# Performance work log

Hardware: AMD Instinct MI355X
Metric: run time of the kernel (lower is better)

The kernel has to match this reference:

```python
import jax, jax.numpy as jnp
import numpy as np

N_NODES = 500_000
N_HYPER = 5_000_000
N_ADJ = 16_000_000


def setup_inputs() -> dict:
    key = jax.random.key(0)
    k1, k2, k3 = jax.random.split(key, 3)
    x = jax.random.uniform(k1, (N_NODES,), dtype=jnp.float32)
    hyper_edges = jax.random.randint(k2, (N_HYPER, 3), 0, N_NODES, dtype=jnp.int32)
    adj_edges = jax.random.randint(k3, (N_ADJ, 2), 0, N_NODES, dtype=jnp.int32)
    return {"x": x, "t": 0, "hyper_edges": hyper_edges, "adj_edges": adj_edges}


def reference(x, t, hyper_edges, adj_edges):
    # x: [N] node states; hyper_edges: [E,3] size-3 hyperedges; adj_edges: [M,2] (src,dst)
    N = x.shape[0]

    # --- hyperedge gather-product-scatter (update_result_3, vectorized) ---
    xe = x[hyper_edges]                       # [E,3] gathered member states
    prod = xe[:, 1] * xe[:, 2]                # product over nodes[1:]
    vals = prod[:, None] - xe * xe            # [E,3] per-member contribution
    hyper_res = jax.ops.segment_sum(
        vals.reshape(-1), hyper_edges.reshape(-1), num_segments=N)

    # --- sparse Laplacian SpMV: L@x = deg*x - A@x (edge-list form) ---
    src = adj_edges[:, 0]
    dst = adj_edges[:, 1]
    Ax = jax.ops.segment_sum(x[src], dst, num_segments=N)
    deg = jax.ops.segment_sum(jnp.ones_like(src, dtype=x.dtype), dst, num_segments=N)
    Lx = deg * x - Ax

    # forward: -0.1 * L@x + 0.9 * hyperedge result
    return -0.1 * Lx + 0.9 * hyper_res
```

## Files before the change

kernel.cpp:

```cpp
#include <hip/hip_runtime.h>
#include <hip/hip_fp16.h>


#define W_BUCKET   8192
#define W_SHIFT    13
#define NB_MAX     62
#define S_STAGE    128
#define A_THREADS  512
#define A_BLOCKS   1024
#define ADJ_TILE   6144
#define HYP_TILE   2048
#define B_PB       16
#define CAP_A      262144
#define CAP_H      245760
#define SRC_MASK   0x7FFFFu

typedef int      v4i __attribute__((ext_vector_type(4)));
typedef unsigned v4u __attribute__((ext_vector_type(4)));
typedef float    v4f __attribute__((ext_vector_type(4)));

#define NT_LOAD(p)     __builtin_nontemporal_load(p)
#define NT_STORE(v, p) __builtin_nontemporal_store((v), (p))


__global__ __launch_bounds__(256) void zero_f4_kernel(float4* __restrict__ p, long long n4) {
    long long tid = (long long)blockIdx.x * blockDim.x + threadIdx.x;
    long long stride = (long long)gridDim.x * blockDim.x;
    for (long long i = tid; i < n4; i += stride) p[i] = make_float4(0.f, 0.f, 0.f, 0.f);
}

__global__ __launch_bounds__(256) void fused_scatter_kernel(
    const float* __restrict__ x, const int2* __restrict__ adj,
    const int* __restrict__ hyper, float* __restrict__ out,
    int n_adj, int n_hyper)
{
    const long long tid = (long long)blockIdx.x * blockDim.x + threadIdx.x;
    const long long stride = (long long)gridDim.x * blockDim.x;
    for (long long i = tid; i < n_adj; i += stride) {
        int2 e = adj[i];
        atomicAdd(&out[e.y], 0.1f * (x[e.x] - x[e.y]));
    }
    for (long long i = tid; i < n_hyper; i += stride) {
        int i0 = hyper[3*i], i1 = hyper[3*i+1], i2 = hyper[3*i+2];
        float x0 = x[i0], x1 = x[i1], x2 = x[i2];
        float p = x1 * x2;
        atomicAdd(&out[i0], 0.9f * (p - x0*x0));
        atomicAdd(&out[i1], 0.9f * (p - x1*x1));
        atomicAdd(&out[i2], 0.9f * (p - x2*x2));
    }
}


__global__ __launch_bounds__(256) void zero_int_kernel(int* __restrict__ p, int n) {
    int tid = blockIdx.x * blockDim.x + threadIdx.x;
    int stride = gridDim.x * blockDim.x;
    for (int i = tid; i < n; i += stride) p[i] = 0;
}


template <int KIND>
__device__ __forceinline__ void flush_stage(int nb, int* cur, int* basev, int* cnts,
                                            unsigned int* stage,
                                            int* __restrict__ g_cursor,
                                            unsigned int* __restrict__ g_records,
                                            long long cap,
                                            const float* __restrict__ x,
                                            float* __restrict__ g_direct,
                                            int wave, int lane, int nwaves) {
    __syncthreads();
    if (wave == 0 && lane < nb) {
        int c = min(cur[lane], S_STAGE);
        cur[lane] = 0;
        int base = 0;
        if (c > 0) base = atomicAdd(&g_cursor[lane], c);
        basev[lane] = base;
        cnts[lane]  = c;
    }
    __syncthreads();
    for (int b = wave; b < nb; b += nwaves) {
        int c = cnts[b];
        long long base = basev[b];
        for (int r = lane; r < c; r += 64) {
            long long idx = base + r;
            unsigned int rec = stage[b * S_STAGE + r];
            if (idx < cap) {
                NT_STORE(rec, &g_records[(long long)b * cap + idx]);
            } else if (KIND == 0) {
                int src = rec & SRC_MASK;
                int dst = b * W_BUCKET + (int)(rec >> 19);
                atomicAdd(&g_direct[dst], 0.1f * (x[src] - x[dst]));
            } else {
                float v = __half2float(__ushort_as_half((unsigned short)(rec & 0xffffu)));
                atomicAdd(&g_direct[b * W_BUCKET + (int)(rec >> 16)], v);
            }
        }
    }
    __syncthreads();
}

__global__ __launch_bounds__(A_THREADS) void binning_kernel(
    const float* __restrict__ x,
    const int*  __restrict__ adj_raw, int n_adj,
    const int*  __restrict__ hyper, int n_hyper,
    int* __restrict__ cur_a, int* __restrict__ cur_h,
    float* __restrict__ g_direct,
    unsigned int* __restrict__ rec_a,
    unsigned int* __restrict__ rec_h,
    int nb)
{
    __shared__ unsigned int stage[NB_MAX * S_STAGE];
    __shared__ int cur[NB_MAX];
    __shared__ int basev[NB_MAX];
    __shared__ int cnts[NB_MAX];

    const int tid = threadIdx.x;
    const int wave = tid >> 6;
    const int lane = tid & 63;
    const int nwaves = A_THREADS >> 6;

    for (int b = tid; b < nb; b += A_THREADS) cur[b] = 0;
    __syncthreads();

    {
        long long per_blk = ((n_adj + A_BLOCKS - 1) / A_BLOCKS + 7) & ~7LL;
        long long a0 = (long long)blockIdx.x * per_blk;
        long long a1 = min((long long)n_adj, a0 + per_blk);
        for (long long t0 = a0; t0 < a1; t0 += ADJ_TILE) {
            long long t1 = min(a1, t0 + ADJ_TILE);
            for (long long g = t0 + (long long)tid * 4; g < t1; g += (long long)A_THREADS * 4) {
                if (g + 4 <= t1) {
                    const v4i* p4 = (const v4i*)(adj_raw + 2 * g);
                    v4i ea = NT_LOAD(p4);
                    v4i eb = NT_LOAD(p4 + 1);
                    int s0 = ea[0], d0 = ea[1],  s1 = ea[2], d1 = ea[3];
                    int s2 = eb[0], d2 = eb[1],  s3 = eb[2], d3 = eb[3];
                    int b0 = d0 >> W_SHIFT, b1 = d1 >> W_SHIFT;
                    int b2 = d2 >> W_SHIFT, b3 = d3 >> W_SHIFT;
                    int p0 = atomicAdd(&cur[b0], 1);
                    int p1 = atomicAdd(&cur[b1], 1);
                    int p2 = atomicAdd(&cur[b2], 1);
                    int p3 = atomicAdd(&cur[b3], 1);
                    if (p0 < S_STAGE) stage[b0*S_STAGE+p0] = ((unsigned)(d0 & (W_BUCKET-1)) << 19) | (unsigned)s0;
                    else atomicAdd(&g_direct[d0], 0.1f * (x[s0] - x[d0]));
                    if (p1 < S_STAGE) stage[b1*S_STAGE+p1] = ((unsigned)(d1 & (W_BUCKET-1)) << 19) | (unsigned)s1;
                    else atomicAdd(&g_direct[d1], 0.1f * (x[s1] - x[d1]));
                    if (p2 < S_STAGE) stage[b2*S_STAGE+p2] = ((unsigned)(d2 & (W_BUCKET-1)) << 19) | (unsigned)s2;
                    else atomicAdd(&g_direct[d2], 0.1f * (x[s2] - x[d2]));
                    if (p3 < S_STAGE) stage[b3*S_STAGE+p3] = ((unsigned)(d3 & (W_BUCKET-1)) << 19) | (unsigned)s3;
                    else atomicAdd(&g_direct[d3], 0.1f * (x[s3] - x[d3]));
                } else {
                    for (long long i = g; i < t1; ++i) {
                        int s = adj_raw[2*i], d = adj_raw[2*i+1];
                        int b = d >> W_SHIFT;
                        int p = atomicAdd(&cur[b], 1);
                        if (p < S_STAGE) stage[b*S_STAGE+p] = ((unsigned)(d & (W_BUCKET-1)) << 19) | (unsigned)s;
                        else atomicAdd(&g_direct[d], 0.1f * (x[s] - x[d]));
                    }
                }
            }
            flush_stage<0>(nb, cur, basev, cnts, stage, cur_a, rec_a, CAP_A,
                           x, g_direct, wave, lane, nwaves);
        }
    }

    {
        long long per_blk = ((n_hyper + A_BLOCKS - 1) / A_BLOCKS + 7) & ~7LL;
        long long h0 = (long long)blockIdx.x * per_blk;
        long long h1 = min((long long)n_hyper, h0 + per_blk);
        for (long long t0 = h0; t0 < h1; t0 += HYP_TILE) {
            long long t1 = min(h1, t0 + HYP_TILE);
            for (long long g = t0 + (long long)tid * 4; g < t1; g += (long long)A_THREADS * 4) {
                if (g + 4 <= t1) {
                    const v4i* p4 = (const v4i*)(hyper + 3 * g);
                    v4i w0 = NT_LOAD(p4);
                    v4i w1 = NT_LOAD(p4 + 1);
                    v4i w2 = NT_LOAD(p4 + 2);
                    int idx[12] = { w0[0], w0[1], w0[2],  w0[3], w1[0], w1[1],
                                    w1[2], w1[3], w2[0],  w2[1], w2[2], w2[3] };
                    float xv[12];
                    #pragma unroll
                    for (int k = 0; k < 12; ++k) xv[k] = x[idx[k]];
                    #pragma unroll
                    for (int e = 0; e < 4; ++e) {
                        float xa = xv[3*e], xb = xv[3*e+1], xc = xv[3*e+2];
                        float pr = xb * xc;
                        int ia = idx[3*e], ib = idx[3*e+1], ic = idx[3*e+2];
                        int ba = ia >> W_SHIFT, bb = ib >> W_SHIFT, bc = ic >> W_SHIFT;
                        int pa = atomicAdd(&cur[ba], 1);
                        int pb = atomicAdd(&cur[bb], 1);
                        int pc = atomicAdd(&cur[bc], 1);
                        float va = 0.9f * (pr - xa*xa);
                        float vb = 0.9f * (pr - xb*xb);
                        float vc = 0.9f * (pr - xc*xc);
                        if (pa < S_STAGE) stage[ba*S_STAGE+pa] = ((unsigned)(ia & (W_BUCKET-1)) << 16) | (unsigned)__half_as_ushort(__float2half(va));
                        else atomicAdd(&g_direct[ia], va);
                        if (pb < S_STAGE) stage[bb*S_STAGE+pb] = ((unsigned)(ib & (W_BUCKET-1)) << 16) | (unsigned)__half_as_ushort(__float2half(vb));
                        else atomicAdd(&g_direct[ib], vb);
                        if (pc < S_STAGE) stage[bc*S_STAGE+pc] = ((unsigned)(ic & (W_BUCKET-1)) << 16) | (unsigned)__half_as_ushort(__float2half(vc));
                        else atomicAdd(&g_direct[ic], vc);
                    }
                } else {
                    for (long long i = g; i < t1; ++i) {
                        int i0 = hyper[3*i], i1 = hyper[3*i+1], i2 = hyper[3*i+2];
                        float x0 = x[i0], x1 = x[i1], x2 = x[i2];
                        float pr = x1 * x2;
                        int b0 = i0 >> W_SHIFT, b1 = i1 >> W_SHIFT, b2 = i2 >> W_SHIFT;
                        int p0 = atomicAdd(&cur[b0], 1);
                        int p1 = atomicAdd(&cur[b1], 1);
                        int p2 = atomicAdd(&cur[b2], 1);
                        float v0 = 0.9f * (pr - x0*x0);
                        float v1 = 0.9f * (pr - x1*x1);
                        float v2 = 0.9f * (pr - x2*x2);
                        if (p0 < S_STAGE) stage[b0*S_STAGE+p0] = ((unsigned)(i0 & (W_BUCKET-1)) << 16) | (unsigned)__half_as_ushort(__float2half(v0));
                        else atomicAdd(&g_direct[i0], v0);
                        if (p1 < S_STAGE) stage[b1*S_STAGE+p1] = ((unsigned)(i1 & (W_BUCKET-1)) << 16) | (unsigned)__half_as_ushort(__float2half(v1));
                        else atomicAdd(&g_direct[i1], v1);
                        if (p2 < S_STAGE) stage[b2*S_STAGE+p2] = ((unsigned)(i2 & (W_BUCKET-1)) << 16) | (unsigned)__half_as_ushort(__float2half(v2));
                        else atomicAdd(&g_direct[i2], v2);
                    }
                }
            }
            flush_stage<1>(nb, cur, basev, cnts, stage, cur_h, rec_h, CAP_H,
                           x, g_direct, wave, lane, nwaves);
        }
    }
}


__global__ __launch_bounds__(512) void accumulate_kernel(
    const float* __restrict__ x,
    const unsigned int* __restrict__ rec_a,
    const unsigned int* __restrict__ rec_h,
    const int* __restrict__ cur_a,
    const int* __restrict__ cur_h,
    float* __restrict__ partials, int n_nodes)
{
    __shared__ float  acc[W_BUCKET];
    __shared__ __half xs[W_BUCKET];
    const int b = blockIdx.x / B_PB;
    const int j = blockIdx.x % B_PB;
    const int base_node = b * W_BUCKET;

    for (int i = threadIdx.x; i < W_BUCKET; i += 512) {
        acc[i] = 0.f;
        int n = base_node + i;
        xs[i] = __float2half(n < n_nodes ? x[n] : 0.f);
    }
    __syncthreads();

    {
        long long cnt = min((long long)cur_a[b], (long long)CAP_A);
        long long g8 = (cnt + 7) >> 3;
        long long s8 = g8 * j / B_PB, e8 = g8 * (j + 1) / B_PB;
        const v4u* r4 = (const v4u*)(rec_a + (long long)b * CAP_A);
        long long i8 = s8 + threadIdx.x;
        v4u r0 = {0,0,0,0}, r1 = {0,0,0,0};
        if (i8 < e8) { r0 = NT_LOAD(r4 + 2*i8); r1 = NT_LOAD(r4 + 2*i8 + 1); }
        while (i8 < e8) {
            long long nx = i8 + 512;
            v4u n0 = {0,0,0,0}, n1 = {0,0,0,0};
            if (nx < e8) { n0 = NT_LOAD(r4 + 2*nx); n1 = NT_LOAD(r4 + 2*nx + 1); }
            long long base = i8 << 3;
            unsigned rr[8] = { r0[0], r0[1], r0[2], r0[3], r1[0], r1[1], r1[2], r1[3] };
            if (base + 7 < cnt) {
                float xv[8];
                #pragma unroll
                for (int k = 0; k < 8; ++k) xv[k] = x[rr[k] & SRC_MASK];
                #pragma unroll
                for (int k = 0; k < 8; ++k) {
                    int dl = rr[k] >> 19;
                    unsafeAtomicAdd(&acc[dl], 0.1f * (xv[k] - __half2float(xs[dl])));
                }
            } else {
                #pragma unroll
                for (int k = 0; k < 8; ++k) {
                    if (base + k < cnt) {
                        int dl = rr[k] >> 19;
                        unsafeAtomicAdd(&acc[dl],
                            0.1f * (x[rr[k] & SRC_MASK] - __half2float(xs[dl])));
                    }
                }
            }
            r0 = n0; r1 = n1; i8 = nx;
        }
    }

    {
        long long cnt = min((long long)cur_h[b], (long long)CAP_H);
        long long g8 = (cnt + 7) >> 3;
        long long s8 = g8 * j / B_PB, e8 = g8 * (j + 1) / B_PB;
        const v4u* r4 = (const v4u*)(rec_h + (long long)b * CAP_H);
        long long i8 = s8 + threadIdx.x;
        v4u r0 = {0,0,0,0}, r1 = {0,0,0,0};
        if (i8 < e8) { r0 = NT_LOAD(r4 + 2*i8); r1 = NT_LOAD(r4 + 2*i8 + 1); }
        while (i8 < e8) {
            long long nx = i8 + 512;
            v4u n0 = {0,0,0,0}, n1 = {0,0,0,0};
            if (nx < e8) { n0 = NT_LOAD(r4 + 2*nx); n1 = NT_LOAD(r4 + 2*nx + 1); }
            long long base = i8 << 3;
            unsigned rr[8] = { r0[0], r0[1], r0[2], r0[3], r1[0], r1[1], r1[2], r1[3] };
            #pragma unroll
            for (int k = 0; k < 8; ++k) {
                if (base + k < cnt) {
                    float v = __half2float(__ushort_as_half((unsigned short)(rr[k] & 0xffffu)));
                    unsafeAtomicAdd(&acc[rr[k] >> 16], v);
                }
            }
            r0 = n0; r1 = n1; i8 = nx;
        }
    }
    __syncthreads();

    float* p = partials + (long long)blockIdx.x * W_BUCKET;
    for (int i = threadIdx.x * 4; i < W_BUCKET; i += 512 * 4) {
        v4f v = { acc[i], acc[i+1], acc[i+2], acc[i+3] };
        NT_STORE(v, (v4f*)(p + i));
    }
}


__global__ __launch_bounds__(256) void finalize_kernel(
    const float* __restrict__ partials,
    const float* __restrict__ g_direct,
    float* __restrict__ out, int n_nodes)
{
    int tid = blockIdx.x * blockDim.x + threadIdx.x;
    int stride = gridDim.x * blockDim.x;
    int n4 = n_nodes >> 2;
    for (int q = tid; q < n4; q += stride) {
        int n = q << 2;
        int b = n >> W_SHIFT, l = n & (W_BUCKET - 1);
        const float* pB = partials + ((long long)b * B_PB) * W_BUCKET + l;
        v4f s = NT_LOAD((const v4f*)(g_direct + n));
        #pragma unroll
        for (int jj = 0; jj < B_PB; ++jj) {
            v4f pv = NT_LOAD((const v4f*)(pB + (long long)jj * W_BUCKET));
            s += pv;
        }
        *(v4f*)(out + n) = s;
    }
}


extern "C" void kernel_launch(void* const* d_in, const int* in_sizes, int n_in,
                              void* d_out, int out_size, void* d_ws, size_t ws_size,
                              hipStream_t stream) {
    const float* x     = (const float*)d_in[0];
    const int*   hyper = (const int*)d_in[2];
    const int*   adj   = (const int*)d_in[3];
    float*       out   = (float*)d_out;

    const int n_nodes = in_sizes[0];
    const int n_hyper = in_sizes[2] / 3;
    const int n_adj   = in_sizes[3] / 2;
    const int nb      = (n_nodes + W_BUCKET - 1) / W_BUCKET;

    const size_t off_cur    = 0;
    const size_t off_direct = 512;
    size_t off_ra = off_direct + (size_t)n_nodes * 4;
    off_ra = (off_ra + 255) & ~(size_t)255;
    const size_t ra_bytes = (size_t)NB_MAX * CAP_A * 4;
    size_t off_rh = off_ra + ra_bytes;
    const size_t rh_bytes = (size_t)NB_MAX * CAP_H * 4;
    size_t off_part = off_rh + rh_bytes;
    off_part = (off_part + 255) & ~(size_t)255;
    const size_t part_bytes = (size_t)NB_MAX * B_PB * W_BUCKET * 4;
    const size_t need = off_part + part_bytes;

    if (nb <= NB_MAX && n_nodes <= (1 << 19) && (n_nodes & 3) == 0 && ws_size >= need) {
        int*          cur_a    = (int*)          ((char*)d_ws + off_cur);
        int*          cur_h    = (int*)          ((char*)d_ws + off_cur + 256);
        float*        g_direct = (float*)        ((char*)d_ws + off_direct);
        unsigned int* rec_a    = (unsigned int*) ((char*)d_ws + off_ra);
        unsigned int* rec_h    = (unsigned int*) ((char*)d_ws + off_rh);
        float*        partials = (float*)        ((char*)d_ws + off_part);

        zero_int_kernel<<<256, 256, 0, stream>>>((int*)d_ws, (int)(off_ra / 4));

        binning_kernel<<<A_BLOCKS, A_THREADS, 0, stream>>>(
            x, adj, n_adj, hyper, n_hyper, cur_a, cur_h, g_direct, rec_a, rec_h, nb);

        accumulate_kernel<<<nb * B_PB, 512, 0, stream>>>(
            x, rec_a, rec_h, cur_a, cur_h, partials, n_nodes);

        finalize_kernel<<<512, 256, 0, stream>>>(partials, g_direct, out, n_nodes);
    } else {
        zero_f4_kernel<<<512, 256, 0, stream>>>((float4*)out, n_nodes / 4);
        fused_scatter_kernel<<<2048, 256, 0, stream>>>(x, (const int2*)adj, hyper, out,
                                                       n_adj, n_hyper);
    }
}
```

Baseline: 514.2 us.

## Pack adjacency sum and degree into one fixed-point integer LDS atomic

Replaces the per-edge float LDS atomic (which also read a half-precision copy of x[dst]) with an integer atomicAdd of a packed word. The high 6 bits count degree and the low 26 bits hold a fixed-point sum of 0.1*x[src]. A conversion pass after the adjacency phase turns the packed word into s - 0.1*deg*x[dst] before the hyperedge float atomics run. The next-record prefetch is also moved to after the gathers are issued. The cost is quantization error and possible overflow if a bucket's degree exceeds 63 or its fixed-point sum exceeds 2^26. An extra sync and LDS pass are added.

```diff
diff --git a/kernel.cpp b/kernel.cpp
--- a/kernel.cpp
+++ b/kernel.cpp
@@ -235,17 +235,13 @@
     const int* __restrict__ cur_h,
     float* __restrict__ partials, int n_nodes)
 {
-    __shared__ float  acc[W_BUCKET];
-    __shared__ __half xs[W_BUCKET];
+    __shared__ unsigned int accu[W_BUCKET];
+    float* accf = (float*)accu;
     const int b = blockIdx.x / B_PB;
     const int j = blockIdx.x % B_PB;
     const int base_node = b * W_BUCKET;
 
-    for (int i = threadIdx.x; i < W_BUCKET; i += 512) {
-        acc[i] = 0.f;
-        int n = base_node + i;
-        xs[i] = __float2half(n < n_nodes ? x[n] : 0.f);
-    }
+    for (int i = threadIdx.x; i < W_BUCKET; i += 512) accu[i] = 0u;
     __syncthreads();
 
     {
@@ -258,32 +254,47 @@
         if (i8 < e8) { r0 = NT_LOAD(r4 + 2*i8); r1 = NT_LOAD(r4 + 2*i8 + 1); }
         while (i8 < e8) {
             long long nx = i8 + 512;
-            v4u n0 = {0,0,0,0}, n1 = {0,0,0,0};
-            if (nx < e8) { n0 = NT_LOAD(r4 + 2*nx); n1 = NT_LOAD(r4 + 2*nx + 1); }
             long long base = i8 << 3;
             unsigned rr[8] = { r0[0], r0[1], r0[2], r0[3], r1[0], r1[1], r1[2], r1[3] };
             if (base + 7 < cnt) {
                 float xv[8];
                 #pragma unroll
                 for (int k = 0; k < 8; ++k) xv[k] = x[rr[k] & SRC_MASK];
+                v4u n0 = {0,0,0,0}, n1 = {0,0,0,0};
+                if (nx < e8) { n0 = NT_LOAD(r4 + 2*nx); n1 = NT_LOAD(r4 + 2*nx + 1); }
                 #pragma unroll
                 for (int k = 0; k < 8; ++k) {
-                    int dl = rr[k] >> 19;
-                    unsafeAtomicAdd(&acc[dl], 0.1f * (xv[k] - __half2float(xs[dl])));
+                    unsigned pv = (1u << 26) + (unsigned)(xv[k] * 104857.6f + 0.5f);
+                    atomicAdd(&accu[rr[k] >> 19], pv);
                 }
+                r0 = n0; r1 = n1;
             } else {
+                v4u n0 = {0,0,0,0}, n1 = {0,0,0,0};
+                if (nx < e8) { n0 = NT_LOAD(r4 + 2*nx); n1 = NT_LOAD(r4 + 2*nx + 1); }
                 #pragma unroll
                 for (int k = 0; k < 8; ++k) {
                     if (base + k < cnt) {
-                        int dl = rr[k] >> 19;
-                        unsafeAtomicAdd(&acc[dl],
-                            0.1f * (x[rr[k] & SRC_MASK] - __half2float(xs[dl])));
+                        float xv = x[rr[k] & SRC_MASK];
+                        unsigned pv = (1u << 26) + (unsigned)(xv * 104857.6f + 0.5f);
+                        atomicAdd(&accu[rr[k] >> 19], pv);
                     }
                 }
+                r0 = n0; r1 = n1;
             }
-            r0 = n0; r1 = n1; i8 = nx;
-        }
-    }
+            i8 = nx;
+        }
+    }
+    __syncthreads();
+
+    for (int i = threadIdx.x; i < W_BUCKET; i += 512) {
+        unsigned p = accu[i];
+        int n = base_node + i;
+        float xn = (n < n_nodes) ? x[n] : 0.f;
+        float s = (float)(p & 0x03FFFFFFu) * (1.0f / 1048576.0f);
+        float deg = (float)(p >> 26);
+        accf[i] = s - 0.1f * deg * xn;
+    }
+    __syncthreads();
 
     {
         long long cnt = min((long long)cur_h[b], (long long)CAP_H);
@@ -303,7 +314,7 @@
             for (int k = 0; k < 8; ++k) {
                 if (base + k < cnt) {
                     float v = __half2float(__ushort_as_half((unsigned short)(rr[k] & 0xffffu)));
-                    unsafeAtomicAdd(&acc[rr[k] >> 16], v);
+                    unsafeAtomicAdd(&accf[rr[k] >> 16], v);
                 }
             }
             r0 = n0; r1 = n1; i8 = nx;
@@ -313,7 +324,7 @@
 
     float* p = partials + (long long)blockIdx.x * W_BUCKET;
     for (int i = threadIdx.x * 4; i < W_BUCKET; i += 512 * 4) {
-        v4f v = { acc[i], acc[i+1], acc[i+2], acc[i+3] };
+        v4f v = { accf[i], accf[i+1], accf[i+2], accf[i+3] };
         NT_STORE(v, (v4f*)(p + i));
     }
 }
```

After: 490.0 us. 4.7% less time.
